# Optimization experiments

Hardware: AMD Instinct MI355X
Metric: run time of the kernel (lower is better)

The kernel has to match this reference:

```python
import jax, jax.numpy as jnp
import numpy as np

N, E = 4096, 131072
IN_DIM, HID, H = 128, 64, 8
D = HID * H          # 512 = d_model
DFF = HID * 4        # 256 (source uses hidden_dim*4, not d_model*4)
NEG_SLOPE = 0.2
LN_EPS = 1e-5


def setup_inputs() -> dict:
    key = jax.random.key(0)
    ks = jax.random.split(key, 24)
    r = lambda i, shp, s=0.05: (jax.random.normal(ks[i], shp, jnp.float32) * s)
    return {
        "x": jax.random.normal(ks[0], (N, IN_DIM), jnp.float32),
        "edge_index": jax.random.randint(ks[1], (2, E), 0, N, dtype=jnp.int32),
        "batch": jnp.zeros((N,), jnp.int32),
        "gat_lin_w": r(2, (D, IN_DIM)),
        "gat_att_src": r(3, (H, HID)),
        "gat_att_dst": r(4, (H, HID)),
        "gat_bias": jnp.zeros((D,), jnp.float32),
        "qkv_w": r(5, (2, 3 * D, D)),
        "qkv_b": jnp.zeros((2, 3 * D), jnp.float32),
        "out_w": r(6, (2, D, D)),
        "out_b": jnp.zeros((2, D), jnp.float32),
        "ln1_g": jnp.ones((2, D), jnp.float32),
        "ln1_b": jnp.zeros((2, D), jnp.float32),
        "ff1_w": r(7, (2, DFF, D)),
        "ff1_b": jnp.zeros((2, DFF), jnp.float32),
        "ff2_w": r(8, (2, D, DFF)),
        "ff2_b": jnp.zeros((2, D), jnp.float32),
        "ln2_g": jnp.ones((2, D), jnp.float32),
        "ln2_b": jnp.zeros((2, D), jnp.float32),
    }


def _layer_norm(x, g, b):
    mu = jnp.mean(x, -1, keepdims=True)
    var = jnp.mean(jnp.square(x - mu), -1, keepdims=True)
    return (x - mu) * jax.lax.rsqrt(var + LN_EPS) * g + b


def _gat(x, edge_index, lin_w, att_src, att_dst, bias):
    # PyG GATConv: linear -> per-edge leaky_relu attention -> softmax over dst -> scatter-add
    h = (x @ lin_w.T).reshape(N, H, HID)                 # [N,H,C]
    loops = jnp.arange(N, dtype=edge_index.dtype)        # add_self_loops=True (PyG default)
    src = jnp.concatenate([edge_index[0], loops])
    dst = jnp.concatenate([edge_index[1], loops])
    a_src = jnp.einsum('nhc,hc->nh', h, att_src)         # [N,H]
    a_dst = jnp.einsum('nhc,hc->nh', h, att_dst)
    e = jax.nn.leaky_relu(a_src[src] + a_dst[dst], NEG_SLOPE)   # [E+N,H]
    emax = jax.ops.segment_max(e, dst, num_segments=N)          # self-loops => no empty segment
    p = jnp.exp(e - emax[dst])
    denom = jax.ops.segment_sum(p, dst, num_segments=N)
    alpha = p / (denom[dst] + 1e-16)                             # [E+N,H]
    msg = alpha[..., None] * h[src]                              # [E+N,H,C]
    out = jax.ops.segment_sum(msg, dst, num_segments=N)         # [N,H,C]
    return out.reshape(N, D) + bias


def _mha(x, w_qkv, b_qkv, w_o, b_o):
    qkv = x @ w_qkv.T + b_qkv                            # [N,3D]
    q, k, v = jnp.split(qkv, 3, axis=-1)
    q = q.reshape(N, H, HID).transpose(1, 0, 2)          # [H,N,c]
    k = k.reshape(N, H, HID).transpose(1, 0, 2)
    v = v.reshape(N, H, HID).transpose(1, 0, 2)
    scores = jnp.einsum('hnc,hmc->hnm', q, k) / jnp.sqrt(jnp.float32(HID))
    attn = jax.nn.softmax(scores, axis=-1)
    o = jnp.einsum('hnm,hmc->hnc', attn, v).transpose(1, 0, 2).reshape(N, D)
    return o @ w_o.T + b_o


def reference(x, edge_index, batch, gat_lin_w, gat_att_src, gat_att_dst, gat_bias,
              qkv_w, qkv_b, out_w, out_b, ln1_g, ln1_b,
              ff1_w, ff1_b, ff2_w, ff2_b, ln2_g, ln2_b):
    h = _gat(x, edge_index, gat_lin_w, gat_att_src, gat_att_dst, gat_bias)
    # TransformerEncoder, 2 post-norm layers, relu FFN, dropout=0; seq_len=N, batch=1
    for i in range(2):
        a = _mha(h, qkv_w[i], qkv_b[i], out_w[i], out_b[i])
        h = _layer_norm(h + a, ln1_g[i], ln1_b[i])
        f = jax.nn.relu(h @ ff1_w[i].T + ff1_b[i]) @ ff2_w[i].T + ff2_b[i]
        h = _layer_norm(h + f, ln2_g[i], ln2_b[i])
    return h
```

## Files before the change

### kernel.cpp

```cpp
#include <hip/hip_runtime.h>
#include <math.h>

#define NN    4096
#define EE    131072
#define ENE   (EE + NN)
#define IND   128
#define HH    8
#define HIDC  64
#define DD    512
#define D3    1536
#define DFF2  256

typedef __attribute__((ext_vector_type(8))) short short8;
typedef __attribute__((ext_vector_type(4))) float f32x4;
typedef __attribute__((ext_vector_type(2))) unsigned int uint2v;

__device__ __forceinline__ float lrelu02(float x) { return x >= 0.f ? x : 0.2f * x; }

__device__ __forceinline__ unsigned short f2bf(float x) {
    unsigned int u = __float_as_uint(x);
    u += 0x7fffu + ((u >> 16) & 1u);
    return (unsigned short)(u >> 16);
}
__device__ __forceinline__ float bf2f(unsigned short u) {
    return __uint_as_float((unsigned int)u << 16);
}
__device__ __forceinline__ unsigned int cvt_pk_bf16(float lo, float hi) {
    unsigned int r;
    asm("v_cvt_pk_bf16_f32 %0, %1, %2" : "=v"(r) : "v"(lo), "v"(hi));
    return r;
}
__device__ __forceinline__ float max3f(float a, float b, float c) {
    float r;
    asm("v_max3_f32 %0, %1, %2, %3" : "=v"(r) : "v"(a), "v"(b), "v"(c));
    return r;
}

struct CvtJobs {
    const float* src[6];
    unsigned short* dst[6];
    int n[6];
};

__global__ __launch_bounds__(256) void cvt_many(CvtJobs jb, int total)
{
    int i = (blockIdx.x * 256 + threadIdx.x) * 4;
    if (i >= total) return;
    int s = 0;
    while (i >= jb.n[s]) { i -= jb.n[s]; ++s; }
    float4 v = *(const float4*)(jb.src[s] + i);
    unsigned int lo = (unsigned int)f2bf(v.x) | ((unsigned int)f2bf(v.y) << 16);
    unsigned int hi = (unsigned int)f2bf(v.z) | ((unsigned int)f2bf(v.w) << 16);
    uint2v pk; pk.x = lo; pk.y = hi;
    *(uint2v*)(jb.dst[s] + i) = pk;
}

__global__ __launch_bounds__(256) void gemm64(const unsigned short* __restrict__ A,
                                              const unsigned short* __restrict__ W,
                                              const float* __restrict__ bias,
                                              void* __restrict__ C,
                                              int M, int K, int N, int flags)
{
    __shared__ __align__(16) unsigned short As[64 * 64];
    __shared__ __align__(16) unsigned short Bs[64 * 64];

    const int t = threadIdx.x, lane = t & 63, w = t >> 6;
    const int wr = w >> 1, wc = w & 1;
    const int bm = blockIdx.y * 64, bn = blockIdx.x * 64;
    const int q = lane & 15, g = lane >> 4;

    f32x4 acc[2][2];
#pragma unroll
    for (int m = 0; m < 2; ++m)
#pragma unroll
        for (int n = 0; n < 2; ++n) acc[m][n] = (f32x4){0.f, 0.f, 0.f, 0.f};

    const int srow = t >> 2, sh = t & 3;
    const unsigned short* Ag = A + (size_t)(bm + srow) * K + sh * 16;
    const unsigned short* Wg = W + (size_t)(bn + srow) * K + sh * 16;
    int wofs[2];
#pragma unroll
    for (int i = 0; i < 2; ++i)
        wofs[i] = srow * 128 + ((((sh * 2 + i) * 16) ^ ((srow & 7) << 4)));

    for (int k0 = 0; k0 < K; k0 += 64) {
        short8 av[2], bv[2];
#pragma unroll
        for (int i = 0; i < 2; ++i) {
            av[i] = *(const short8*)(Ag + k0 + i * 8);
            bv[i] = *(const short8*)(Wg + k0 + i * 8);
        }
        __syncthreads();
#pragma unroll
        for (int i = 0; i < 2; ++i) {
            *(short8*)((char*)As + wofs[i]) = av[i];
            *(short8*)((char*)Bs + wofs[i]) = bv[i];
        }
        __syncthreads();

        short8 af[2][2], bfr[2][2];
#pragma unroll
        for (int m = 0; m < 2; ++m) {
            const int row = wr * 32 + m * 16 + q;
#pragma unroll
            for (int kk = 0; kk < 2; ++kk)
                af[kk][m] = *(const short8*)((const char*)As +
                    row * 128 + ((((kk * 4 + g) * 16) ^ ((row & 7) << 4))));
        }
#pragma unroll
        for (int n = 0; n < 2; ++n) {
            const int row = wc * 32 + n * 16 + q;
#pragma unroll
            for (int kk = 0; kk < 2; ++kk)
                bfr[kk][n] = *(const short8*)((const char*)Bs +
                    row * 128 + ((((kk * 4 + g) * 16) ^ ((row & 7) << 4))));
        }
#pragma unroll
        for (int kk = 0; kk < 2; ++kk)
#pragma unroll
            for (int m = 0; m < 2; ++m)
#pragma unroll
                for (int n = 0; n < 2; ++n)
                    acc[m][n] = __builtin_amdgcn_mfma_f32_16x16x32_bf16(
                        bfr[kk][n], af[kk][m], acc[m][n], 0, 0, 0);
    }

    const int obf = flags & 1, orelu = flags & 2, oqs = flags & 4;
#pragma unroll
    for (int m = 0; m < 2; ++m) {
        const int row = bm + wr * 32 + m * 16 + q;
#pragma unroll
        for (int n = 0; n < 2; ++n) {
            const int col0 = bn + wc * 32 + n * 16 + g * 4;
            f32x4 v = acc[m][n];
            if (bias) {
                float4 bv4 = *(const float4*)(bias + col0);
                v[0] += bv4.x; v[1] += bv4.y; v[2] += bv4.z; v[3] += bv4.w;
            }
            if (oqs && col0 < DD) {
                const float qs = 0.18033688f;
                v[0] *= qs; v[1] *= qs; v[2] *= qs; v[3] *= qs;
            }
            if (orelu) {
                v[0] = fmaxf(v[0], 0.f); v[1] = fmaxf(v[1], 0.f);
                v[2] = fmaxf(v[2], 0.f); v[3] = fmaxf(v[3], 0.f);
            }
            if (obf) {
                uint2v pk;
                pk.x = (unsigned int)f2bf(v[0]) | ((unsigned int)f2bf(v[1]) << 16);
                pk.y = (unsigned int)f2bf(v[2]) | ((unsigned int)f2bf(v[3]) << 16);
                *(uint2v*)((unsigned short*)C + (size_t)row * N + col0) = pk;
            } else {
                float4 o; o.x = v[0]; o.y = v[1]; o.z = v[2]; o.w = v[3];
                *(float4*)((float*)C + (size_t)row * N + col0) = o;
            }
        }
    }
}

__global__ void att_proj(const unsigned short* __restrict__ hlin,
                         const float* __restrict__ att_s,
                         const float* __restrict__ att_d,
                         float* __restrict__ a_src, float* __restrict__ a_dst)
{
    int idx = blockIdx.x * 256 + threadIdx.x;
    if (idx >= NN * HH) return;
    int n = idx >> 3, h = idx & 7;
    const unsigned short* hp = hlin + (size_t)n * DD + h * HIDC;
    const float* as = att_s + h * HIDC;
    const float* ad = att_d + h * HIDC;
    float s1 = 0.f, s2 = 0.f;
#pragma unroll 8
    for (int c = 0; c < HIDC; ++c) {
        float hv = bf2f(hp[c]);
        s1 += hv * as[c]; s2 += hv * ad[c];
    }
    a_src[idx] = s1;
    a_dst[idx] = s2;
}

__global__ void hist_kernel(const int* __restrict__ ei, int* __restrict__ counts)
{
    int i = blockIdx.x * 256 + threadIdx.x;
    if (i >= ENE) return;
    int dst = (i < EE) ? ei[EE + i] : (i - EE);
    atomicAdd(&counts[dst], 1);
}

__global__ __launch_bounds__(1024) void scan_kernel(const int* __restrict__ counts,
                                                    int* __restrict__ offsets)
{
    __shared__ int sums[1024];
    int t = threadIdx.x;
    int v0 = counts[t*4+0], v1 = counts[t*4+1], v2 = counts[t*4+2], v3 = counts[t*4+3];
    sums[t] = v0 + v1 + v2 + v3;
    __syncthreads();
    for (int off = 1; off < 1024; off <<= 1) {
        int x = (t >= off) ? sums[t - off] : 0;
        __syncthreads();
        sums[t] += x;
        __syncthreads();
    }
    int pre = (t > 0) ? sums[t-1] : 0;
    offsets[t*4+0] = pre;
    offsets[t*4+1] = pre + v0;
    offsets[t*4+2] = pre + v0 + v1;
    offsets[t*4+3] = pre + v0 + v1 + v2;
    if (t == 1023) offsets[4096] = sums[1023];
}

__global__ void scatter_kernel(const int* __restrict__ ei, const int* __restrict__ offs,
                               int* __restrict__ cursor, int* __restrict__ src_sorted)
{
    int i = blockIdx.x * 256 + threadIdx.x;
    if (i >= ENE) return;
    int s, d;
    if (i < EE) { s = ei[i]; d = ei[EE + i]; } else { s = d = i - EE; }
    int pos = atomicAdd(&cursor[d], 1);
    src_sorted[offs[d] + pos] = s;
}

__global__ __launch_bounds__(256) void gat_node(const unsigned short* __restrict__ hlin,
                                                const float* __restrict__ a_src,
                                                const float* __restrict__ a_dst,
                                                const int* __restrict__ offs,
                                                const int* __restrict__ src_sorted,
                                                const float* __restrict__ bias,
                                                float* __restrict__ out,
                                                unsigned short* __restrict__ outb)
{
    __shared__ float adst[8];
    __shared__ float emax[8];
    __shared__ float denom[8];
    __shared__ float red[256];
    __shared__ float p_lds[16][8];
    __shared__ int   srcs[16];

    const int n = blockIdx.x, t = threadIdx.x;
    if (t < 8) { adst[t] = a_dst[n * 8 + t]; denom[t] = 0.f; }
    const int off0 = offs[n];
    const int deg  = offs[n+1] - off0;
    __syncthreads();

    const int h = t & 7, slot = t >> 3;
    float mx = -3.0e38f;
    for (int j = slot; j < deg; j += 32) {
        int s = src_sorted[off0 + j];
        mx = fmaxf(mx, a_src[s * 8 + h] + adst[h]);
    }
    red[t] = mx;
    __syncthreads();
    for (int half = 128; half >= 8; half >>= 1) {
        if (t < half) red[t] = fmaxf(red[t], red[t + half]);
        __syncthreads();
    }
    if (t < 8) emax[t] = lrelu02(red[t]);
    __syncthreads();

    float acc0 = 0.f, acc1 = 0.f;
    const int c0 = 2 * t;
    const int hh = t >> 5;
    for (int base = 0; base < deg; base += 16) {
        int cnt = min(16, deg - base);
        if (t < cnt * 8) {
            int j = base + (t >> 3);
            int s = src_sorted[off0 + j];
            if ((t & 7) == 0) srcs[t >> 3] = s;
            float x = a_src[s * 8 + (t & 7)] + adst[t & 7];
            float p = __expf(lrelu02(x) - emax[t & 7]);
            p_lds[t >> 3][t & 7] = p;
            atomicAdd(&denom[t & 7], p);
        }
        __syncthreads();
        for (int jj = 0; jj < cnt; ++jj) {
            int s = srcs[jj];
            unsigned int hv = *(const unsigned int*)(hlin + (size_t)s * DD + c0);
            float p = p_lds[jj][hh];
            acc0 += p * bf2f((unsigned short)(hv & 0xffffu));
            acc1 += p * bf2f((unsigned short)(hv >> 16));
        }
        __syncthreads();
    }
    const float dinv = 1.f / (denom[hh] + 1e-16f);
    float o0 = acc0 * dinv + bias[c0];
    float o1 = acc1 * dinv + bias[c0 + 1];
    float2 ov; ov.x = o0; ov.y = o1;
    *(float2*)(out + (size_t)n * DD + c0) = ov;
    unsigned int pk = (unsigned int)f2bf(o0) | ((unsigned int)f2bf(o1) << 16);
    *(unsigned int*)(outb + (size_t)n * DD + c0) = pk;
}

#define KVB 128
#define NTT (NN / KVB)

__global__ __launch_bounds__(256) void attn_mfma(const unsigned short* __restrict__ qkv,
                                                 unsigned short* __restrict__ aob)
{
    __shared__ __align__(16) unsigned short Ks0[KVB * 64];
    __shared__ __align__(16) unsigned short Vt0[80 * KVB];
    __shared__ __align__(16) unsigned short Ks1[KVB * 64];
    __shared__ __align__(16) unsigned short Vt1[80 * KVB];

    const int t = threadIdx.x;
    const int w = t >> 6, lane = t & 63;
    const int q15 = lane & 15, g = lane >> 4;

    const int fid = blockIdx.x;
    const int h = fid & 7, qb = fid >> 3;
    const int qbase = qb * 64 + w * 16;

    const unsigned short* qrow = qkv + (size_t)(qbase + q15) * D3 + h * HIDC;
    const short8 qf0 = *(const short8*)(qrow + g * 8);
    const short8 qf1 = *(const short8*)(qrow + 32 + g * 8);

    f32x4 O[4];
#pragma unroll
    for (int db = 0; db < 4; ++db) O[db] = (f32x4){0.f, 0.f, 0.f, 0.f};
    f32x4 O5 = (f32x4){0.f, 0.f, 0.f, 0.f};
    float m_run = -3.0e38f;

    int koff[8][2];
#pragma unroll
    for (int kvb = 0; kvb < 8; ++kvb) {
        const int kr = kvb * 16 + q15;
        koff[kvb][0] = (kr * 64 + g * 8) ^ ((kr & 7) << 3);
        koff[kvb][1] = (kr * 64 + 32 + g * 8) ^ ((kr & 7) << 3);
    }
    int voff[4][4];
#pragma unroll
    for (int db = 0; db < 4; ++db) {
        const int vr = db * 16 + q15;
#pragma unroll
        for (int ks = 0; ks < 4; ++ks)
            voff[db][ks] = (vr * KVB + ks * 32 + g * 8) ^ ((vr & 7) << 3);
    }
    int voffE[4];
#pragma unroll
    for (int ks = 0; ks < 4; ++ks) {
        const int rv = 64 + q15;
        voffE[ks] = (rv * KVB + ks * 32 + g * 8) ^ ((rv & 7) << 3);
    }
    const int kr_s = t >> 1, sh = t & 1;
    const int kq = t & 31, dg = t >> 5;
    const int slot4 = (kq >> 3) * 32 + (kq & 3) * 8 + ((kq >> 2) & 1) * 4;
    int kwoff[4];
#pragma unroll
    for (int i = 0; i < 4; ++i)
        kwoff[i] = (kr_s * 64 + (sh * 4 + i) * 8) ^ ((kr_s & 7) << 3);
    int vwoff[8];
#pragma unroll
    for (int i = 0; i < 8; ++i) {
        const int d = dg * 8 + i;
        vwoff[i] = (d * KVB + slot4) ^ ((d & 7) << 3);
    }
    const unsigned short* Kg = qkv + (size_t)kr_s * D3 + DD + h * HIDC + sh * 32;
    const unsigned short* Vg = qkv + (size_t)(4 * kq) * D3 + 2 * DD + h * HIDC + dg * 8;

    short8 kreg[4], vreg[4];

    auto LOAD_KV = [&](int kb) {
        const size_t off = (size_t)kb * KVB * D3;
#pragma unroll
        for (int i = 0; i < 4; ++i) kreg[i] = *(const short8*)(Kg + off + i * 8);
#pragma unroll
        for (int jj = 0; jj < 4; ++jj) vreg[jj] = *(const short8*)(Vg + off + (size_t)jj * D3);
    };
    auto WRITE_KV = [&](unsigned short* KD, unsigned short* VD) {
#pragma unroll
        for (int i = 0; i < 4; ++i)
            *(short8*)&KD[kwoff[i]] = kreg[i];
        const unsigned int* w0 = (const unsigned int*)&vreg[0];
        const unsigned int* w1 = (const unsigned int*)&vreg[1];
        const unsigned int* w2 = (const unsigned int*)&vreg[2];
        const unsigned int* w3 = (const unsigned int*)&vreg[3];
#pragma unroll
        for (int i = 0; i < 8; ++i) {
            const unsigned int sel = (i & 1) ? 0x07060302u : 0x05040100u;
            uint2v pk;
            pk.x = __builtin_amdgcn_perm(w1[i >> 1], w0[i >> 1], sel);
            pk.y = __builtin_amdgcn_perm(w3[i >> 1], w2[i >> 1], sel);
            *(uint2v*)&VD[vwoff[i]] = pk;
        }
    };

    auto TILE = [&](int kb, const unsigned short* BK, const unsigned short* BV,
                    unsigned short* NK, unsigned short* NV) {
        const int kbn = kb + 1;
        if (kbn < NTT) LOAD_KV(kbn);

        f32x4 st[8];
        __builtin_amdgcn_s_setprio(1);
#pragma unroll
        for (int kvb = 0; kvb < 8; ++kvb) {
            const short8 kf0 = *(const short8*)&BK[koff[kvb][0]];
            const short8 kf1 = *(const short8*)&BK[koff[kvb][1]];
            f32x4 acc = (f32x4){0.f, 0.f, 0.f, 0.f};
            acc = __builtin_amdgcn_mfma_f32_16x16x32_bf16(kf0, qf0, acc, 0, 0, 0);
            acc = __builtin_amdgcn_mfma_f32_16x16x32_bf16(kf1, qf1, acc, 0, 0, 0);
            st[kvb] = acc;
        }
        __builtin_amdgcn_s_setprio(0);

        float pm0 = max3f(st[0][0], st[0][1], st[0][2]);
        float pm1 = max3f(st[0][3], st[1][0], st[1][1]);
        float pm2 = max3f(st[1][2], st[1][3], st[2][0]);
        float pm3 = max3f(st[2][1], st[2][2], st[2][3]);
        float pm4 = max3f(st[3][0], st[3][1], st[3][2]);
        float pm5 = max3f(st[3][3], st[4][0], st[4][1]);
        float pm6 = max3f(st[4][2], st[4][3], st[5][0]);
        float pm7 = max3f(st[5][1], st[5][2], st[5][3]);
        float pm8 = max3f(st[6][0], st[6][1], st[6][2]);
        float pm9 = max3f(st[6][3], st[7][0], st[7][1]);
        float pmA = max3f(st[7][2], st[7][3], pm0);
        float q0 = max3f(pm1, pm2, pm3);
        float q1 = max3f(pm4, pm5, pm6);
        float q2 = max3f(pm7, pm8, pm9);
        float pmax = max3f(q0, q1, q2);
        pmax = fmaxf(pmax, pmA);
        pmax = fmaxf(pmax, __shfl_xor(pmax, 16, 64));
        pmax = fmaxf(pmax, __shfl_xor(pmax, 32, 64));
        if (!__all(pmax <= m_run + 11.f)) {
            const float mnew = fmaxf(m_run, pmax);
            const float f = exp2f(m_run - mnew);
#pragma unroll
            for (int db = 0; db < 4; ++db) O[db] *= f;
            O5 *= f;
            m_run = mnew;
        }

        short8 pf[4];
#pragma unroll
        for (int ks = 0; ks < 4; ++ks) {
            float e0 = exp2f(st[2*ks  ][0] - m_run), e1 = exp2f(st[2*ks  ][1] - m_run);
            float e2 = exp2f(st[2*ks  ][2] - m_run), e3 = exp2f(st[2*ks  ][3] - m_run);
            float e4 = exp2f(st[2*ks+1][0] - m_run), e5 = exp2f(st[2*ks+1][1] - m_run);
            float e6 = exp2f(st[2*ks+1][2] - m_run), e7 = exp2f(st[2*ks+1][3] - m_run);
            union { unsigned int u[4]; short8 s8; } pu;
            pu.u[0] = cvt_pk_bf16(e0, e1);
            pu.u[1] = cvt_pk_bf16(e2, e3);
            pu.u[2] = cvt_pk_bf16(e4, e5);
            pu.u[3] = cvt_pk_bf16(e6, e7);
            pf[ks] = pu.s8;
        }

        __builtin_amdgcn_s_setprio(1);
#pragma unroll
        for (int db = 0; db < 4; ++db) {
#pragma unroll
            for (int ks = 0; ks < 4; ++ks) {
                const short8 vf = *(const short8*)&BV[voff[db][ks]];
                O[db] = __builtin_amdgcn_mfma_f32_16x16x32_bf16(vf, pf[ks], O[db], 0, 0, 0);
            }
        }
#pragma unroll
        for (int ks = 0; ks < 4; ++ks) {
            const short8 vfE = *(const short8*)&BV[voffE[ks]];
            O5 = __builtin_amdgcn_mfma_f32_16x16x32_bf16(vfE, pf[ks], O5, 0, 0, 0);
        }
        __builtin_amdgcn_s_setprio(0);

        if (kbn < NTT) {
            WRITE_KV(NK, NV);
            __syncthreads();
        }
    };

    {
        const int d = 64 + (t >> 4), c = (t & 15) * 8;
        short8 iv;
#pragma unroll
        for (int i = 0; i < 8; ++i)
            iv[i] = (short)((d == 64) ? 0x3F80 : 0);
        const int ofs = (d * KVB + c) ^ ((d & 7) << 3);
        *(short8*)&Vt0[ofs] = iv;
        *(short8*)&Vt1[ofs] = iv;
    }
    LOAD_KV(0);
    WRITE_KV(Ks0, Vt0);
    __syncthreads();

    for (int kb = 0; kb < NTT; kb += 2) {
        TILE(kb,     Ks0, Vt0, Ks1, Vt1);
        TILE(kb + 1, Ks1, Vt1, Ks0, Vt0);
    }

    const float lsum = __shfl(O5[0], q15, 64);
    const float linv = 1.f / lsum;
#pragma unroll
    for (int db = 0; db < 4; ++db) {
        uint2v pk;
        pk.x = (unsigned int)f2bf(O[db][0] * linv) | ((unsigned int)f2bf(O[db][1] * linv) << 16);
        pk.y = (unsigned int)f2bf(O[db][2] * linv) | ((unsigned int)f2bf(O[db][3] * linv) << 16);
        *(uint2v*)&aob[(size_t)(qbase + q15) * DD + h * HIDC + db * 16 + g * 4] = pk;
    }
}

__global__ __launch_bounds__(256) void ln_fused(const float* __restrict__ hin,
                                                const unsigned short* __restrict__ dlt,
                                                const float* __restrict__ g,
                                                const float* __restrict__ b,
                                                float* __restrict__ out,
                                                unsigned short* __restrict__ outb)
{
    __shared__ float red[256];
    const int r = blockIdx.x, t = threadIdx.x;
    const size_t base = (size_t)r * DD;
    float2 hv = *(const float2*)(hin + base + 2 * t);
    unsigned int dv = *(const unsigned int*)(dlt + base + 2 * t);
    float v0 = hv.x + bf2f((unsigned short)(dv & 0xffffu));
    float v1 = hv.y + bf2f((unsigned short)(dv >> 16));
    red[t] = v0 + v1;
    __syncthreads();
    for (int off = 128; off > 0; off >>= 1) { if (t < off) red[t] += red[t + off]; __syncthreads(); }
    float mu = red[0] * (1.f / 512.f);
    __syncthreads();
    float d0 = v0 - mu, d1 = v1 - mu;
    red[t] = d0 * d0 + d1 * d1;
    __syncthreads();
    for (int off = 128; off > 0; off >>= 1) { if (t < off) red[t] += red[t + off]; __syncthreads(); }
    float rs = rsqrtf(red[0] * (1.f / 512.f) + 1e-5f);
    float2 gv = *(const float2*)(g + 2 * t);
    float2 bv = *(const float2*)(b + 2 * t);
    float o0 = d0 * rs * gv.x + bv.x;
    float o1 = d1 * rs * gv.y + bv.y;
    float2 ov; ov.x = o0; ov.y = o1;
    *(float2*)(out + base + 2 * t) = ov;
    if (outb) {
        unsigned int pk = (unsigned int)f2bf(o0) | ((unsigned int)f2bf(o1) << 16);
        *(unsigned int*)(outb + base + 2 * t) = pk;
    }
}

extern "C" void kernel_launch(void* const* d_in, const int* in_sizes, int n_in,
                              void* d_out, int out_size, void* d_ws, size_t ws_size,
                              hipStream_t stream)
{
    (void)in_sizes; (void)n_in; (void)out_size; (void)ws_size;

    const float* x        = (const float*)d_in[0];
    const int*   ei       = (const int*)  d_in[1];
    const float* lin_w    = (const float*)d_in[3];
    const float* att_src  = (const float*)d_in[4];
    const float* att_dst  = (const float*)d_in[5];
    const float* gat_bias = (const float*)d_in[6];
    const float* qkv_w    = (const float*)d_in[7];
    const float* qkv_b    = (const float*)d_in[8];
    const float* out_w    = (const float*)d_in[9];
    const float* out_b    = (const float*)d_in[10];
    const float* ln1_g    = (const float*)d_in[11];
    const float* ln1_b    = (const float*)d_in[12];
    const float* ff1_w    = (const float*)d_in[13];
    const float* ff1_b    = (const float*)d_in[14];
    const float* ff2_w    = (const float*)d_in[15];
    const float* ff2_b    = (const float*)d_in[16];
    const float* ln2_g    = (const float*)d_in[17];
    const float* ln2_b    = (const float*)d_in[18];

    char* wsb = (char*)d_ws;
    size_t o = 0;
    auto alloc = [&](size_t bytes) { char* p = wsb + o; o += (bytes + 255) & ~(size_t)255; return p; };

    unsigned short* hlin_bf = (unsigned short*)alloc((size_t)NN * DD * 2);
    unsigned short* hbf     = (unsigned short*)alloc((size_t)NN * DD * 2);
    unsigned short* qkv16   = (unsigned short*)alloc((size_t)NN * D3 * 2);
    unsigned short* aob     = (unsigned short*)alloc((size_t)NN * DD * 2);
    unsigned short* ff1obf  = (unsigned short*)alloc((size_t)NN * DFF2 * 2);
    unsigned short* dltbf   = (unsigned short*)alloc((size_t)NN * DD * 2);
    float* hcur  = (float*)alloc((size_t)NN * DD * 4);
    float* a_src = (float*)alloc((size_t)NN * HH * 4);
    float* a_dst = (float*)alloc((size_t)NN * HH * 4);
    int* counts     = (int*)alloc(NN * 4);
    int* cursor     = (int*)alloc(NN * 4);
    int* offsets    = (int*)alloc((NN + 1) * 4);
    int* src_sorted = (int*)alloc(ENE * 4);
    unsigned short* xbf    = (unsigned short*)alloc((size_t)NN * IND * 2);
    unsigned short* linwbf = (unsigned short*)alloc((size_t)DD * IND * 2);
    unsigned short* qkvwbf = (unsigned short*)alloc((size_t)2 * D3 * DD * 2);
    unsigned short* outwbf = (unsigned short*)alloc((size_t)2 * DD * DD * 2);
    unsigned short* ff1wbf = (unsigned short*)alloc((size_t)2 * DFF2 * DD * 2);
    unsigned short* ff2wbf = (unsigned short*)alloc((size_t)2 * DD * DFF2 * 2);

    CvtJobs jb;
    jb.src[0] = x;      jb.dst[0] = xbf;    jb.n[0] = NN * IND;
    jb.src[1] = lin_w;  jb.dst[1] = linwbf; jb.n[1] = DD * IND;
    jb.src[2] = qkv_w;  jb.dst[2] = qkvwbf; jb.n[2] = 2 * D3 * DD;
    jb.src[3] = out_w;  jb.dst[3] = outwbf; jb.n[3] = 2 * DD * DD;
    jb.src[4] = ff1_w;  jb.dst[4] = ff1wbf; jb.n[4] = 2 * DFF2 * DD;
    jb.src[5] = ff2_w;  jb.dst[5] = ff2wbf; jb.n[5] = 2 * DD * DFF2;
    int cvt_total = jb.n[0]+jb.n[1]+jb.n[2]+jb.n[3]+jb.n[4]+jb.n[5];
    cvt_many<<<(cvt_total/4 + 255)/256, 256, 0, stream>>>(jb, cvt_total);

    hipMemsetAsync(counts, 0, 2 * NN * sizeof(int), stream);
    gemm64<<<dim3(DD/64, NN/64), 256, 0, stream>>>(xbf, linwbf, nullptr, hlin_bf,
                                                   NN, IND, DD, 1);
    att_proj<<<(NN*HH + 255)/256, 256, 0, stream>>>(hlin_bf, att_src, att_dst, a_src, a_dst);
    hist_kernel<<<(ENE + 255)/256, 256, 0, stream>>>(ei, counts);
    scan_kernel<<<1, 1024, 0, stream>>>(counts, offsets);
    scatter_kernel<<<(ENE + 255)/256, 256, 0, stream>>>(ei, offsets, cursor, src_sorted);
    gat_node<<<NN, 256, 0, stream>>>(hlin_bf, a_src, a_dst, offsets, src_sorted, gat_bias,
                                     hcur, hbf);

    for (int i = 0; i < 2; ++i) {
        gemm64<<<dim3(D3/64, NN/64), 256, 0, stream>>>(hbf, qkvwbf + (size_t)i*D3*DD,
                                                       qkv_b + (size_t)i*D3, qkv16,
                                                       NN, DD, D3, 1 | 4);
        attn_mfma<<<dim3(NN/64 * HH), 256, 0, stream>>>(qkv16, aob);
        gemm64<<<dim3(DD/64, NN/64), 256, 0, stream>>>(aob, outwbf + (size_t)i*DD*DD,
                                                       out_b + (size_t)i*DD, dltbf,
                                                       NN, DD, DD, 1);
        ln_fused<<<NN, 256, 0, stream>>>(hcur, dltbf, ln1_g + (size_t)i*DD, ln1_b + (size_t)i*DD,
                                         hcur, hbf);
        gemm64<<<dim3(DFF2/64, NN/64), 256, 0, stream>>>(hbf, ff1wbf + (size_t)i*DFF2*DD,
                                                         ff1_b + (size_t)i*DFF2, ff1obf,
                                                         NN, DD, DFF2, 1 | 2);
        gemm64<<<dim3(DD/64, NN/64), 256, 0, stream>>>(ff1obf, ff2wbf + (size_t)i*DD*DFF2,
                                                       ff2_b + (size_t)i*DD, dltbf,
                                                       NN, DFF2, DD, 1);
        float* outp = (i == 1) ? (float*)d_out : hcur;
        unsigned short* outbp = (i == 1) ? nullptr : hbf;
        ln_fused<<<NN, 256, 0, stream>>>(hcur, dltbf, ln2_g + (size_t)i*DD, ln2_b + (size_t)i*DD,
                                         outp, outbp);
    }
}
```

Measured before the change: 329.2 us.

## Split attention KV range in two and merge partials in a combine kernel

The attention kernel now splits the 4096 keys into two halves handled by separate blocks, doubling the grid from 512 to 1024 blocks, and shrinks the KV tile from 128 to 64 rows. Each block writes an unnormalized bf16 partial output plus its running max and sum, and a new combine kernel rescales and merges the two halves. The aim is better occupancy and CU utilisation on a grid that was too small for the device. The cost is an extra launch, extra global traffic for the partial outputs, and an additional bf16 rounding of the unnormalized partials.

```diff
diff --git a/kernel.cpp b/kernel.cpp
--- a/kernel.cpp
+++ b/kernel.cpp
@@ -12,6 +12,7 @@
 #define DFF2  256
 
 typedef __attribute__((ext_vector_type(8))) short short8;
+typedef __attribute__((ext_vector_type(4))) short short4v;
 typedef __attribute__((ext_vector_type(4))) float f32x4;
 typedef __attribute__((ext_vector_type(2))) unsigned int uint2v;
 
@@ -290,11 +291,13 @@
     *(unsigned int*)(outb + (size_t)n * DD + c0) = pk;
 }
 
-#define KVB 128
-#define NTT (NN / KVB)
+#define KVB   64
+#define SPLIT 2
+#define NTS   ((NN / SPLIT) / KVB)
 
 __global__ __launch_bounds__(256) void attn_mfma(const unsigned short* __restrict__ qkv,
-                                                 unsigned short* __restrict__ aob)
+                                                 unsigned short* __restrict__ po,
+                                                 float2* __restrict__ ml)
 {
     __shared__ __align__(16) unsigned short Ks0[KVB * 64];
     __shared__ __align__(16) unsigned short Vt0[80 * KVB];
@@ -306,8 +309,9 @@
     const int q15 = lane & 15, g = lane >> 4;
 
     const int fid = blockIdx.x;
-    const int h = fid & 7, qb = fid >> 3;
+    const int h = fid & 7, s = (fid >> 3) & 1, qb = fid >> 4;
     const int qbase = qb * 64 + w * 16;
+    const int kv0 = s * (NN / SPLIT);
 
     const unsigned short* qrow = qkv + (size_t)(qbase + q15) * D3 + h * HIDC;
     const short8 qf0 = *(const short8*)(qrow + g * 8);
@@ -319,66 +323,67 @@
     f32x4 O5 = (f32x4){0.f, 0.f, 0.f, 0.f};
     float m_run = -3.0e38f;
 
-    int koff[8][2];
-#pragma unroll
-    for (int kvb = 0; kvb < 8; ++kvb) {
+    int koff[4][2];
+#pragma unroll
+    for (int kvb = 0; kvb < 4; ++kvb) {
         const int kr = kvb * 16 + q15;
         koff[kvb][0] = (kr * 64 + g * 8) ^ ((kr & 7) << 3);
         koff[kvb][1] = (kr * 64 + 32 + g * 8) ^ ((kr & 7) << 3);
     }
-    int voff[4][4];
+    int voff[4][2];
 #pragma unroll
     for (int db = 0; db < 4; ++db) {
         const int vr = db * 16 + q15;
 #pragma unroll
-        for (int ks = 0; ks < 4; ++ks)
+        for (int ks = 0; ks < 2; ++ks)
             voff[db][ks] = (vr * KVB + ks * 32 + g * 8) ^ ((vr & 7) << 3);
     }
-    int voffE[4];
-#pragma unroll
-    for (int ks = 0; ks < 4; ++ks) {
+    int voffE[2];
+#pragma unroll
+    for (int ks = 0; ks < 2; ++ks) {
         const int rv = 64 + q15;
         voffE[ks] = (rv * KVB + ks * 32 + g * 8) ^ ((rv & 7) << 3);
     }
-    const int kr_s = t >> 1, sh = t & 1;
-    const int kq = t & 31, dg = t >> 5;
+    const int kr_s = t >> 2, sh = t & 3;
+    const int kq = t & 15, dg = t >> 4;
     const int slot4 = (kq >> 3) * 32 + (kq & 3) * 8 + ((kq >> 2) & 1) * 4;
-    int kwoff[4];
-#pragma unroll
-    for (int i = 0; i < 4; ++i)
-        kwoff[i] = (kr_s * 64 + (sh * 4 + i) * 8) ^ ((kr_s & 7) << 3);
-    int vwoff[8];
-#pragma unroll
-    for (int i = 0; i < 8; ++i) {
-        const int d = dg * 8 + i;
+    int kwoff[2];
+#pragma unroll
+    for (int i = 0; i < 2; ++i)
+        kwoff[i] = (kr_s * 64 + (sh * 2 + i) * 8) ^ ((kr_s & 7) << 3);
+    int vwoff[4];
+#pragma unroll
+    for (int i = 0; i < 4; ++i) {
+        const int d = dg * 4 + i;
         vwoff[i] = (d * KVB + slot4) ^ ((d & 7) << 3);
     }
-    const unsigned short* Kg = qkv + (size_t)kr_s * D3 + DD + h * HIDC + sh * 32;
-    const unsigned short* Vg = qkv + (size_t)(4 * kq) * D3 + 2 * DD + h * HIDC + dg * 8;
-
-    short8 kreg[4], vreg[4];
+    const unsigned short* Kg = qkv + (size_t)(kv0 + kr_s) * D3 + DD + h * HIDC + sh * 16;
+    const unsigned short* Vg = qkv + (size_t)(kv0 + 4 * kq) * D3 + 2 * DD + h * HIDC + dg * 4;
+
+    short8 kreg[2];
+    short4v vr4[4];
 
     auto LOAD_KV = [&](int kb) {
         const size_t off = (size_t)kb * KVB * D3;
 #pragma unroll
-        for (int i = 0; i < 4; ++i) kreg[i] = *(const short8*)(Kg + off + i * 8);
-#pragma unroll
-        for (int jj = 0; jj < 4; ++jj) vreg[jj] = *(const short8*)(Vg + off + (size_t)jj * D3);
+        for (int i = 0; i < 2; ++i) kreg[i] = *(const short8*)(Kg + off + i * 8);
+#pragma unroll
+        for (int j = 0; j < 4; ++j) vr4[j] = *(const short4v*)(Vg + off + (size_t)j * D3);
     };
     auto WRITE_KV = [&](unsigned short* KD, unsigned short* VD) {
 #pragma unroll
-        for (int i = 0; i < 4; ++i)
+        for (int i = 0; i < 2; ++i)
             *(short8*)&KD[kwoff[i]] = kreg[i];
-        const unsigned int* w0 = (const unsigned int*)&vreg[0];
-        const unsigned int* w1 = (const unsigned int*)&vreg[1];
-        const unsigned int* w2 = (const unsigned int*)&vreg[2];
-        const unsigned int* w3 = (const unsigned int*)&vreg[3];
-#pragma unroll
-        for (int i = 0; i < 8; ++i) {
+        const unsigned int* u0 = (const unsigned int*)&vr4[0];
+        const unsigned int* u1 = (const unsigned int*)&vr4[1];
+        const unsigned int* u2 = (const unsigned int*)&vr4[2];
+        const unsigned int* u3 = (const unsigned int*)&vr4[3];
+#pragma unroll
+        for (int i = 0; i < 4; ++i) {
             const unsigned int sel = (i & 1) ? 0x07060302u : 0x05040100u;
             uint2v pk;
-            pk.x = __builtin_amdgcn_perm(w1[i >> 1], w0[i >> 1], sel);
-            pk.y = __builtin_amdgcn_perm(w3[i >> 1], w2[i >> 1], sel);
+            pk.x = __builtin_amdgcn_perm(u1[i >> 1], u0[i >> 1], sel);
+            pk.y = __builtin_amdgcn_perm(u3[i >> 1], u2[i >> 1], sel);
             *(uint2v*)&VD[vwoff[i]] = pk;
         }
     };
@@ -386,12 +391,12 @@
     auto TILE = [&](int kb, const unsigned short* BK, const unsigned short* BV,
                     unsigned short* NK, unsigned short* NV) {
         const int kbn = kb + 1;
-        if (kbn < NTT) LOAD_KV(kbn);
-
-        f32x4 st[8];
+        if (kbn < NTS) LOAD_KV(kbn);
+
+        f32x4 st[4];
         __builtin_amdgcn_s_setprio(1);
 #pragma unroll
-        for (int kvb = 0; kvb < 8; ++kvb) {
+        for (int kvb = 0; kvb < 4; ++kvb) {
             const short8 kf0 = *(const short8*)&BK[koff[kvb][0]];
             const short8 kf1 = *(const short8*)&BK[koff[kvb][1]];
             f32x4 acc = (f32x4){0.f, 0.f, 0.f, 0.f};
@@ -406,17 +411,9 @@
         float pm2 = max3f(st[1][2], st[1][3], st[2][0]);
         float pm3 = max3f(st[2][1], st[2][2], st[2][3]);
         float pm4 = max3f(st[3][0], st[3][1], st[3][2]);
-        float pm5 = max3f(st[3][3], st[4][0], st[4][1]);
-        float pm6 = max3f(st[4][2], st[4][3], st[5][0]);
-        float pm7 = max3f(st[5][1], st[5][2], st[5][3]);
-        float pm8 = max3f(st[6][0], st[6][1], st[6][2]);
-        float pm9 = max3f(st[6][3], st[7][0], st[7][1]);
-        float pmA = max3f(st[7][2], st[7][3], pm0);
-        float q0 = max3f(pm1, pm2, pm3);
-        float q1 = max3f(pm4, pm5, pm6);
-        float q2 = max3f(pm7, pm8, pm9);
-        float pmax = max3f(q0, q1, q2);
-        pmax = fmaxf(pmax, pmA);
+        float r0 = max3f(pm0, pm1, pm2);
+        float r1 = max3f(pm3, pm4, st[3][3]);
+        float pmax = fmaxf(r0, r1);
         pmax = fmaxf(pmax, __shfl_xor(pmax, 16, 64));
         pmax = fmaxf(pmax, __shfl_xor(pmax, 32, 64));
         if (!__all(pmax <= m_run + 11.f)) {
@@ -428,9 +425,9 @@
             m_run = mnew;
         }
 
-        short8 pf[4];
-#pragma unroll
-        for (int ks = 0; ks < 4; ++ks) {
+        short8 pf[2];
+#pragma unroll
+        for (int ks = 0; ks < 2; ++ks) {
             float e0 = exp2f(st[2*ks  ][0] - m_run), e1 = exp2f(st[2*ks  ][1] - m_run);
             float e2 = exp2f(st[2*ks  ][2] - m_run), e3 = exp2f(st[2*ks  ][3] - m_run);
             float e4 = exp2f(st[2*ks+1][0] - m_run), e5 = exp2f(st[2*ks+1][1] - m_run);
@@ -447,52 +444,81 @@
 #pragma unroll
         for (int db = 0; db < 4; ++db) {
 #pragma unroll
-            for (int ks = 0; ks < 4; ++ks) {
+            for (int ks = 0; ks < 2; ++ks) {
                 const short8 vf = *(const short8*)&BV[voff[db][ks]];
                 O[db] = __builtin_amdgcn_mfma_f32_16x16x32_bf16(vf, pf[ks], O[db], 0, 0, 0);
             }
         }
 #pragma unroll
-        for (int ks = 0; ks < 4; ++ks) {
+        for (int ks = 0; ks < 2; ++ks) {
             const short8 vfE = *(const short8*)&BV[voffE[ks]];
             O5 = __builtin_amdgcn_mfma_f32_16x16x32_bf16(vfE, pf[ks], O5, 0, 0, 0);
         }
         __builtin_amdgcn_s_setprio(0);
 
-        if (kbn < NTT) {
+        if (kbn < NTS) {
             WRITE_KV(NK, NV);
             __syncthreads();
         }
     };
 
     {
-        const int d = 64 + (t >> 4), c = (t & 15) * 8;
-        short8 iv;
-#pragma unroll
-        for (int i = 0; i < 8; ++i)
+        const int d = 64 + (t >> 4), c = (t & 15) * 4;
+        short4v iv;
+#pragma unroll
+        for (int i = 0; i < 4; ++i)
             iv[i] = (short)((d == 64) ? 0x3F80 : 0);
         const int ofs = (d * KVB + c) ^ ((d & 7) << 3);
-        *(short8*)&Vt0[ofs] = iv;
-        *(short8*)&Vt1[ofs] = iv;
+        *(short4v*)&Vt0[ofs] = iv;
+        *(short4v*)&Vt1[ofs] = iv;
     }
     LOAD_KV(0);
     WRITE_KV(Ks0, Vt0);
     __syncthreads();
 
-    for (int kb = 0; kb < NTT; kb += 2) {
+    for (int kb = 0; kb < NTS; kb += 2) {
         TILE(kb,     Ks0, Vt0, Ks1, Vt1);
         TILE(kb + 1, Ks1, Vt1, Ks0, Vt0);
     }
 
-    const float lsum = __shfl(O5[0], q15, 64);
-    const float linv = 1.f / lsum;
+    const size_t prow = (size_t)s * NN + qbase + q15;
 #pragma unroll
     for (int db = 0; db < 4; ++db) {
         uint2v pk;
-        pk.x = (unsigned int)f2bf(O[db][0] * linv) | ((unsigned int)f2bf(O[db][1] * linv) << 16);
-        pk.y = (unsigned int)f2bf(O[db][2] * linv) | ((unsigned int)f2bf(O[db][3] * linv) << 16);
-        *(uint2v*)&aob[(size_t)(qbase + q15) * DD + h * HIDC + db * 16 + g * 4] = pk;
-    }
+        pk.x = cvt_pk_bf16(O[db][0], O[db][1]);
+        pk.y = cvt_pk_bf16(O[db][2], O[db][3]);
+        *(uint2v*)&po[prow * DD + h * HIDC + db * 16 + g * 4] = pk;
+    }
+    if (lane < 16)
+        ml[prow * HH + h] = make_float2(m_run, O5[0]);
+}
+
+__global__ __launch_bounds__(256) void attn_combine(const unsigned short* __restrict__ po,
+                                                    const float2* __restrict__ ml,
+                                                    unsigned short* __restrict__ aob)
+{
+    int idx = blockIdx.x * 256 + threadIdx.x;
+    if (idx >= NN * DD / 4) return;
+    int q = idx >> 7;
+    int rem = idx & 127;
+    int h = rem >> 4;
+    int col = rem * 4;
+    float2 ml0 = ml[(size_t)q * HH + h];
+    float2 ml1 = ml[((size_t)NN + q) * HH + h];
+    float M  = fmaxf(ml0.x, ml1.x);
+    float f0 = exp2f(ml0.x - M), f1 = exp2f(ml1.x - M);
+    float inv = 1.f / (f0 * ml0.y + f1 * ml1.y);
+    f0 *= inv; f1 *= inv;
+    uint2v o0 = *(const uint2v*)&po[(size_t)q * DD + col];
+    uint2v o1 = *(const uint2v*)&po[(size_t)(NN + q) * DD + col];
+    float r0 = f0 * bf2f((unsigned short)(o0.x & 0xffffu)) + f1 * bf2f((unsigned short)(o1.x & 0xffffu));
+    float r1 = f0 * bf2f((unsigned short)(o0.x >> 16))     + f1 * bf2f((unsigned short)(o1.x >> 16));
+    float r2 = f0 * bf2f((unsigned short)(o0.y & 0xffffu)) + f1 * bf2f((unsigned short)(o1.y & 0xffffu));
+    float r3 = f0 * bf2f((unsigned short)(o0.y >> 16))     + f1 * bf2f((unsigned short)(o1.y >> 16));
+    uint2v pk;
+    pk.x = (unsigned int)f2bf(r0) | ((unsigned int)f2bf(r1) << 16);
+    pk.y = (unsigned int)f2bf(r2) | ((unsigned int)f2bf(r3) << 16);
+    *(uint2v*)&aob[(size_t)q * DD + col] = pk;
 }
 
 __global__ __launch_bounds__(256) void ln_fused(const float* __restrict__ hin,
@@ -566,6 +592,8 @@
     unsigned short* aob     = (unsigned short*)alloc((size_t)NN * DD * 2);
     unsigned short* ff1obf  = (unsigned short*)alloc((size_t)NN * DFF2 * 2);
     unsigned short* dltbf   = (unsigned short*)alloc((size_t)NN * DD * 2);
+    unsigned short* po16    = (unsigned short*)alloc((size_t)SPLIT * NN * DD * 2);
+    float2* mlb             = (float2*)alloc((size_t)SPLIT * NN * HH * 8);
     float* hcur  = (float*)alloc((size_t)NN * DD * 4);
     float* a_src = (float*)alloc((size_t)NN * HH * 4);
     float* a_dst = (float*)alloc((size_t)NN * HH * 4);
@@ -604,7 +632,8 @@
         gemm64<<<dim3(D3/64, NN/64), 256, 0, stream>>>(hbf, qkvwbf + (size_t)i*D3*DD,
                                                        qkv_b + (size_t)i*D3, qkv16,
                                                        NN, DD, D3, 1 | 4);
-        attn_mfma<<<dim3(NN/64 * HH), 256, 0, stream>>>(qkv16, aob);
+        attn_mfma<<<dim3(NN/64 * HH * SPLIT), 256, 0, stream>>>(qkv16, po16, mlb);
+        attn_combine<<<(NN*DD/4 + 255)/256, 256, 0, stream>>>(po16, mlb, aob);
         gemm64<<<dim3(DD/64, NN/64), 256, 0, stream>>>(aob, outwbf + (size_t)i*DD*DD,
                                                        out_b + (size_t)i*DD, dltbf,
                                                        NN, DD, DD, 1);
```

Result: slower. 373.8 us (+13.5%).
